# Performance work log

Hardware: AMD Instinct MI355X
Metric: run time of the kernel (lower is better)

## Reference

```python
import jax, jax.numpy as jnp
import numpy as np

B, S, P, D, H = 2, 1024, 1024, 2048, 16
DH = D // H
QMAX = 127.0


def quantize(x):
    # per-tensor abs-max int8 quantization, matching torch quantize(bits=8)
    scale = jnp.max(jnp.abs(x)) / QMAX
    x_q = jnp.clip(jnp.round(x / scale), -128.0, 127.0).astype(jnp.int8)
    return x_q, scale


def dequantize(x_q, scale):
    return x_q.astype(jnp.float32) * scale


def setup_inputs() -> dict:
    key = jax.random.key(0)
    ks = jax.random.split(key, 12)
    sd = 1.0 / np.sqrt(D)
    inp = {
        'hidden_states': jax.random.normal(ks[0], (B, S, D), jnp.float32),
        'Wq': jax.random.normal(ks[1], (D, D), jnp.float32) * sd,
        'bq': jnp.zeros((D,), jnp.float32),
        'Wk': jax.random.normal(ks[2], (D, D), jnp.float32) * sd,
        'bk': jnp.zeros((D,), jnp.float32),
        'Wv': jax.random.normal(ks[3], (D, D), jnp.float32) * sd,
        'bv': jnp.zeros((D,), jnp.float32),
        'Wo': jax.random.normal(ks[4], (D, D), jnp.float32) * sd,
        'bo': jnp.zeros((D,), jnp.float32),
        'past_k_q': jax.random.randint(ks[5], (B, P, D), -128, 128).astype(jnp.int8),
        'past_k_scale': jnp.float32(0.03),
        'past_v_q': jax.random.randint(ks[6], (B, P, D), -128, 128).astype(jnp.int8),
        'past_v_scale': jnp.float32(0.02),
    }
    return inp


def attention(h, k, v, Wq, bq, Wo, bo):
    # standard causal MHA; query positions are offset by the cache length P
    T = k.shape[1]  # P + S
    q = (h @ Wq + bq).reshape(B, S, H, DH)
    kh = k.reshape(B, T, H, DH)
    vh = v.reshape(B, T, H, DH)
    scores = jnp.einsum('bshd,bthd->bhst', q, kh) / np.sqrt(DH)  # [B,H,S,T]
    causal = jnp.arange(T)[None, :] <= (P + jnp.arange(S))[:, None]  # [S,T]
    scores = jnp.where(causal[None, None], scores, jnp.float32(-1e30))
    attn = jax.nn.softmax(scores, axis=-1)
    out = jnp.einsum('bhst,bthd->bshd', attn, vh).reshape(B, S, D)
    return out @ Wo + bo


def reference(hidden_states, Wq, bq, Wk, bk, Wv, bv, Wo, bo,
              past_k_q, past_k_scale, past_v_q, past_v_scale):
    k = hidden_states @ Wk + bk  # [B,S,D]
    v = hidden_states @ Wv + bv
    k_q, k_scale = quantize(k)
    v_q, v_scale = quantize(v)
    # dequantize cached KV and concat along the sequence dim (dim=1)
    k_prev = dequantize(past_k_q, past_k_scale)
    v_prev = dequantize(past_v_q, past_v_scale)
    k_full = jnp.concatenate([k_prev, k], axis=1)  # [B,P+S,D]
    v_full = jnp.concatenate([v_prev, v], axis=1)
    out = attention(hidden_states, k_full, v_full, Wq, bq, Wo, bo)
    return out, k_q, k_scale, v_q, v_scale
```

## Files before the change

### kernel.cpp

```cpp
#include <hip/hip_runtime.h>

#define SOFT_SCALE 0.08838834764831845f
#define BSD 4194304
#define NELEM 4194304

typedef __attribute__((ext_vector_type(4))) float    f32x4;
typedef __attribute__((ext_vector_type(8))) short    bf16x8;
typedef __attribute__((ext_vector_type(4))) short    bf16x4;
typedef __attribute__((ext_vector_type(4))) unsigned u32x4;

__device__ __forceinline__ float bs2f(short s) {
    unsigned u = ((unsigned)(unsigned short)s) << 16;
    return __builtin_bit_cast(float, u);
}
__device__ __forceinline__ short f2bs(float f) {
    unsigned u = __builtin_bit_cast(unsigned, f);
    unsigned r = (u + 0x7fffu + ((u >> 16) & 1u)) >> 16;
    return (short)r;
}

__device__ __forceinline__ void stage16(const short* g, short* l) {
#if __has_builtin(__builtin_amdgcn_global_load_lds)
    __builtin_amdgcn_global_load_lds(
        (const __attribute__((address_space(1))) void*)g,
        (__attribute__((address_space(3))) void*)l, 16, 0, 0);
#else
    *(bf16x8*)l = *(const bf16x8*)g;
#endif
}

__global__ void probe_init(const int* __restrict__ q, float* __restrict__ scal) {
    const int lane = threadIdx.x;
    int bad = 0;
#pragma unroll
    for (int i = 0; i < 4; ++i) {
        const int v = q[i * 64 + lane];
        bad |= (v < -128 || v > 127) ? 1 : 0;
    }
    const int anybad = __any(bad);
    if (lane == 0) ((int*)scal)[2] = anybad ? 0 : 1;
    if (lane == 1) scal[0] = 0.f;
    if (lane == 2) scal[1] = 0.f;
}

__global__ void prep_kernel(const float* __restrict__ X, short* __restrict__ Y,
                            const void* __restrict__ pk, const void* __restrict__ pv,
                            const float* __restrict__ psk, const float* __restrict__ psv,
                            short* __restrict__ Kf, short* __restrict__ Vf,
                            const int* __restrict__ wsflag) {
    const int z = blockIdx.z;
    const int stride = gridDim.x * blockDim.x;
    if (z == 0) {
        for (int i = blockIdx.x * blockDim.x + threadIdx.x; i < NELEM / 8; i += stride) {
            const int e = i * 8;
            f32x4 a = *(const f32x4*)&X[e];
            f32x4 b = *(const f32x4*)&X[e + 4];
            bf16x8 o;
            o[0] = f2bs(a[0]); o[1] = f2bs(a[1]); o[2] = f2bs(a[2]); o[3] = f2bs(a[3]);
            o[4] = f2bs(b[0]); o[5] = f2bs(b[1]); o[6] = f2bs(b[2]); o[7] = f2bs(b[3]);
            *(bf16x8*)&Y[e] = o;
        }
    } else {
        const void* src = (z == 2) ? pv : pk;
        const float sc = (z == 2) ? *psv : *psk;
        short* dst = (z == 2) ? Vf : Kf;
        const int flag = wsflag[2];
        for (int i = blockIdx.x * blockDim.x + threadIdx.x; i < NELEM / 8; i += stride) {
            const int e = i * 8;
            int vals[8];
            if (flag) {
                const int* s = (const int*)src + e;
                *(int4*)&vals[0] = *(const int4*)&s[0];
                *(int4*)&vals[4] = *(const int4*)&s[4];
            } else {
                const int2 wv = *(const int2*)((const char*)src + e);
#pragma unroll
                for (int j = 0; j < 4; ++j) vals[j] = (int)(signed char)(wv.x >> (8 * j));
#pragma unroll
                for (int j = 0; j < 4; ++j) vals[4 + j] = (int)(signed char)(wv.y >> (8 * j));
            }
            bf16x8 o;
#pragma unroll
            for (int j = 0; j < 8; ++j) o[j] = f2bs((float)vals[j] * sc);
            *(bf16x8*)&dst[e + ((e >> 21) << 21)] = o;
        }
    }
}

__global__ __launch_bounds__(256) void transpose_conv(const float* __restrict__ W0,
                                                      const float* __restrict__ W1,
                                                      const float* __restrict__ W2,
                                                      const float* __restrict__ W3,
                                                      short* __restrict__ WT) {
    __shared__ __align__(16) short Tl[64 * 68];
    const float* W = blockIdx.z == 0 ? W0 : (blockIdx.z == 1 ? W1 :
                     (blockIdx.z == 2 ? W2 : W3));
    short* out = WT + (long)blockIdx.z * 4194304;
    const int tid = threadIdx.x;
    const int n0 = blockIdx.x * 64, k0 = blockIdx.y * 64;
#pragma unroll
    for (int i = 0; i < 4; ++i) {
        const int e = i * 1024 + tid * 4;
        const int r = e >> 6, c = e & 63;
        f32x4 f = *(const f32x4*)&W[(long)(k0 + r) * 2048 + n0 + c];
        bf16x4 s4 = { f2bs(f[0]), f2bs(f[1]), f2bs(f[2]), f2bs(f[3]) };
        *(bf16x4*)&Tl[r * 68 + c] = s4;
    }
    __syncthreads();
#pragma unroll
    for (int i = 0; i < 4; ++i) {
        const int e = i * 1024 + tid * 4;
        const int nr = e >> 6, kk = e & 63;
        bf16x4 o = { Tl[(kk + 0) * 68 + nr], Tl[(kk + 1) * 68 + nr],
                     Tl[(kk + 2) * 68 + nr], Tl[(kk + 3) * 68 + nr] };
        *(bf16x4*)&out[(long)(n0 + nr) * 2048 + k0 + kk] = o;
    }
}

__global__ __launch_bounds__(256, 2) void gemm_m97(
    const short* __restrict__ A,
    const short* __restrict__ Bt0, const short* __restrict__ Bt1, const short* __restrict__ Bt2,
    const float* __restrict__ bi0, const float* __restrict__ bi1, const float* __restrict__ bi2,
    void* __restrict__ o0, void* __restrict__ o1, void* __restrict__ o2,
    int mode_sgl, float scale_sgl) {
    __shared__ __align__(16) short Al[2][4096];
    __shared__ __align__(16) short Bl[2][4096];
    const int nbx = gridDim.x, nby = gridDim.y, nbz = gridDim.z;
    const int nwg = nbx * nby * nbz;
    const int orig = blockIdx.x + nbx * (blockIdx.y + nby * blockIdx.z);
    const int cpx = nwg >> 3;
    int swz = (orig & 7) * cpx + (orig >> 3);
    const int bx = swz % nbx; swz /= nbx;
    const int by = swz % nby;
    const int bz = swz / nby;

    const short* Bt   = bz == 0 ? Bt0 : (bz == 1 ? Bt1 : Bt2);
    const float* bias = bz == 0 ? bi0 : (bz == 1 ? bi1 : bi2);
    void* outp        = bz == 0 ? o0  : (bz == 1 ? o1  : o2);
    int mode; float scl;
    if (nbz == 3) { mode = (bz == 0) ? 1 : 2; scl = (bz == 0) ? SOFT_SCALE : 1.f; }
    else          { mode = mode_sgl;          scl = scale_sgl; }

    const int tid = threadIdx.x, lane = tid & 63, w = tid >> 6;
    const int wm = w >> 1, wn = w & 1, l4 = lane >> 4, ln = lane & 15;
    const int m0 = by * 128, n0 = bx * 128;

    const short* gA0 = A  + (long)(m0 + (tid >> 2)) * 2048 + (tid & 3) * 8;
    const short* gA1 = gA0 + 64 * 2048;
    const short* gB0 = Bt + (long)(n0 + (tid >> 2)) * 2048 + (tid & 3) * 8;
    const short* gB1 = gB0 + 64 * 2048;

    f32x4 acc[4][4];
#pragma unroll
    for (int mi = 0; mi < 4; ++mi)
#pragma unroll
        for (int ni = 0; ni < 4; ++ni) acc[mi][ni] = (f32x4){0, 0, 0, 0};

#define STAGE_G(buf, ko)                                   \
    do {                                                   \
        stage16(gA0 + (ko), &Al[buf][tid * 8]);            \
        stage16(gA1 + (ko), &Al[buf][2048 + tid * 8]);     \
        stage16(gB0 + (ko), &Bl[buf][tid * 8]);            \
        stage16(gB1 + (ko), &Bl[buf][2048 + tid * 8]);     \
    } while (0)

    STAGE_G(0, 0);
    asm volatile("s_waitcnt vmcnt(0)" ::: "memory");
    __syncthreads();
    int cur = 0;
    for (int kt = 0; kt < 64; ++kt) {
        if (kt < 63) STAGE_G(cur ^ 1, (kt + 1) * 32);
        bf16x8 af[4], bfr[4];
#pragma unroll
        for (int mi = 0; mi < 4; ++mi)
            af[mi] = *(const bf16x8*)&Al[cur][(wm * 64 + mi * 16 + ln) * 32 + l4 * 8];
#pragma unroll
        for (int ni = 0; ni < 4; ++ni)
            bfr[ni] = *(const bf16x8*)&Bl[cur][(wn * 64 + ni * 16 + ln) * 32 + l4 * 8];
#pragma unroll
        for (int mi = 0; mi < 4; ++mi)
#pragma unroll
            for (int ni = 0; ni < 4; ++ni)
                acc[mi][ni] = __builtin_amdgcn_mfma_f32_16x16x32_bf16(
                    af[mi], bfr[ni], acc[mi][ni], 0, 0, 0);
        asm volatile("s_waitcnt vmcnt(0)" ::: "memory");
        __syncthreads();
        cur ^= 1;
    }
#undef STAGE_G

#pragma unroll
    for (int ni = 0; ni < 4; ++ni) {
        const int gn = n0 + wn * 64 + ni * 16 + ln;
        const float bv = bias[gn];
#pragma unroll
        for (int mi = 0; mi < 4; ++mi) {
#pragma unroll
            for (int r = 0; r < 4; ++r) {
                const int gm = m0 + wm * 64 + mi * 16 + l4 * 4 + r;
                const float v = (acc[mi][ni][r] + bv) * scl;
                if (mode == 0) {
                    ((float*)outp)[(long)gm * 2048 + gn] = v;
                } else if (mode == 1) {
                    ((short*)outp)[(long)gm * 2048 + gn] = f2bs(v);
                } else {
                    const int gr = gm + 1024 + ((gm >> 10) << 10);
                    ((short*)outp)[(long)gr * 2048 + gn] = f2bs(v);
                }
            }
        }
    }
}

__global__ __launch_bounds__(256, 2) void gemm_wo(const short* __restrict__ A,
                                                  const short* __restrict__ Bt,
                                                  const float* __restrict__ bias,
                                                  float* __restrict__ outp) {
    __shared__ __align__(16) short Al[2][4096];
    __shared__ __align__(16) short Bl[2][2048];
    const int orig = blockIdx.x + 32 * blockIdx.y;
    const int swz = (orig & 7) * 64 + (orig >> 3);
    const int bx = swz & 31, by = swz >> 5;
    const int tid = threadIdx.x, lane = tid & 63, w = tid >> 6;
    const int wm = w >> 1, wn = w & 1, l4 = lane >> 4, ln = lane & 15;
    const int m0 = by * 128, n0 = bx * 64;

    const short* gA0 = A  + (long)(m0 + (tid >> 2)) * 2048 + (tid & 3) * 8;
    const short* gA1 = gA0 + 64 * 2048;
    const short* gB0 = Bt + (long)(n0 + (tid >> 2)) * 2048 + (tid & 3) * 8;

    f32x4 acc[4][2];
#pragma unroll
    for (int mi = 0; mi < 4; ++mi)
#pragma unroll
        for (int ni = 0; ni < 2; ++ni) acc[mi][ni] = (f32x4){0, 0, 0, 0};

#define STAGE_W(buf, ko)                                   \
    do {                                                   \
        stage16(gA0 + (ko), &Al[buf][tid * 8]);            \
        stage16(gA1 + (ko), &Al[buf][2048 + tid * 8]);     \
        stage16(gB0 + (ko), &Bl[buf][tid * 8]);            \
    } while (0)

    STAGE_W(0, 0);
    asm volatile("s_waitcnt vmcnt(0)" ::: "memory");
    __syncthreads();
    int cur = 0;
    for (int kt = 0; kt < 64; ++kt) {
        if (kt < 63) STAGE_W(cur ^ 1, (kt + 1) * 32);
        bf16x8 af[4], bfr[2];
#pragma unroll
        for (int mi = 0; mi < 4; ++mi)
            af[mi] = *(const bf16x8*)&Al[cur][(wm * 64 + mi * 16 + ln) * 32 + l4 * 8];
#pragma unroll
        for (int ni = 0; ni < 2; ++ni)
            bfr[ni] = *(const bf16x8*)&Bl[cur][(wn * 32 + ni * 16 + ln) * 32 + l4 * 8];
#pragma unroll
        for (int mi = 0; mi < 4; ++mi)
#pragma unroll
            for (int ni = 0; ni < 2; ++ni)
                acc[mi][ni] = __builtin_amdgcn_mfma_f32_16x16x32_bf16(
                    af[mi], bfr[ni], acc[mi][ni], 0, 0, 0);
        asm volatile("s_waitcnt vmcnt(0)" ::: "memory");
        __syncthreads();
        cur ^= 1;
    }
#undef STAGE_W

#pragma unroll
    for (int ni = 0; ni < 2; ++ni) {
        const int gn = n0 + wn * 32 + ni * 16 + ln;
        const float bv = bias[gn];
#pragma unroll
        for (int mi = 0; mi < 4; ++mi) {
#pragma unroll
            for (int r = 0; r < 4; ++r) {
                const int gm = m0 + wm * 64 + mi * 16 + l4 * 4 + r;
                outp[(long)gm * 2048 + gn] = acc[mi][ni][r] + bv;
            }
        }
    }
}

__global__ void absmax_kernel(const short* __restrict__ Kf, const short* __restrict__ Vf,
                              float* __restrict__ scal) {
    const int z = blockIdx.z;
    const short* src = z ? Vf : Kf;
    const int tid = threadIdx.x, lane = tid & 63, w = tid >> 6;
    float mx = 0.f;
    const int stride = gridDim.x * blockDim.x;
    for (int i = blockIdx.x * blockDim.x + tid; i < NELEM / 8; i += stride) {
        const int e = i * 8;
        const int flat = e + 2097152 + ((e >> 21) << 21);
        bf16x8 v = *(const bf16x8*)&src[flat];
#pragma unroll
        for (int j = 0; j < 8; ++j) mx = fmaxf(mx, fabsf(bs2f(v[j])));
    }
#pragma unroll
    for (int o = 32; o > 0; o >>= 1) mx = fmaxf(mx, __shfl_xor(mx, o));
    __shared__ float wred[4];
    if (lane == 0) wred[w] = mx;
    __syncthreads();
    if (tid == 0) {
        const float m2 = fmaxf(fmaxf(wred[0], wred[1]), fmaxf(wred[2], wred[3]));
        atomicMax((unsigned int*)&scal[z], __builtin_bit_cast(unsigned int, m2));
    }
}

__global__ void quantize_kernel(const short* __restrict__ Kf, const short* __restrict__ Vf,
                                const float* __restrict__ scal, float* __restrict__ out) {
    const int z = blockIdx.z;
    const short* src = z ? Vf : Kf;
    const float mx = scal[z];
    const float scale = mx * (1.f / 127.f);
    const float inv = (mx > 0.f) ? 127.f / mx : 0.f;
    const long ob = z ? (2L * BSD + 1) : (1L * BSD);
    if (blockIdx.x == 0 && threadIdx.x == 0)
        out[z ? (3L * BSD + 1) : (2L * BSD)] = scale;
    const int stride = gridDim.x * blockDim.x;
    for (int i = blockIdx.x * blockDim.x + threadIdx.x; i < NELEM / 4; i += stride) {
        const int e = i * 4;
        const int flat = e + 2097152 + ((e >> 21) << 21);
        bf16x4 x4 = *(const bf16x4*)&src[flat];
        float4 q;
        q.x = fminf(127.f, fmaxf(-128.f, rintf(bs2f(x4[0]) * inv)));
        q.y = fminf(127.f, fmaxf(-128.f, rintf(bs2f(x4[1]) * inv)));
        q.z = fminf(127.f, fmaxf(-128.f, rintf(bs2f(x4[2]) * inv)));
        q.w = fminf(127.f, fmaxf(-128.f, rintf(bs2f(x4[3]) * inv)));
        *(float4*)&out[ob + e] = q;
    }
}

__global__ __launch_bounds__(256, 2) void attn_kernel(const short* __restrict__ Q,
                                                      const short* __restrict__ Kf,
                                                      const short* __restrict__ Vf,
                                                      short* __restrict__ O) {
    __shared__ __align__(16) short Kl[2][64 * 136];
    __shared__ __align__(16) short Vt[2][128 * 72];
    const int L = blockIdx.x + 16 * (blockIdx.y + 16 * blockIdx.z);
    const int x = L & 7, rr = L >> 3;
    const int qt0 = rr & 15, pgrp = rr >> 4;
    const int p = x + 8 * pgrp;
    const int h = p >> 1, b = p & 1;
    const int qt = (pgrp >= 2) ? (15 - qt0) : qt0;

    const int tid = threadIdx.x, w = tid >> 6, lane = tid & 63;
    const int l4 = lane >> 4, n = lane & 15;
    const int rg = tid >> 4, cg = tid & 15, stc = cg * 8;
    const int sIdx = qt * 64 + w * 16 + n;
    const int qlim = 1024 + sIdx;

    bf16x8 qf[4];
#pragma unroll
    for (int c = 0; c < 4; ++c)
        qf[c] = *(const bf16x8*)&Q[(long)(b * 1024 + sIdx) * 2048 + h * 128 + c * 32 + l4 * 8];

    f32x4 acco[8];
#pragma unroll
    for (int i = 0; i < 8; ++i) acco[i] = (f32x4){0, 0, 0, 0};
    float m_run = 0.f, l_run = 0.f;

    const short* Kb = Kf + (long)(b * 2048) * 2048 + h * 128;
    const short* Vb = Vf + (long)(b * 2048) * 2048 + h * 128;
    const int nt = 17 + qt;

    bf16x8 kreg[4], vreg[4];
#define LOAD_KV(te)                                                                   \
    do {                                                                              \
        _Pragma("unroll")                                                             \
        for (int i = 0; i < 4; ++i)                                                   \
            kreg[i] = *(const bf16x8*)&Kb[(long)((te) + i * 16 + rg) * 2048 + stc];   \
        _Pragma("unroll")                                                             \
        for (int i = 0; i < 4; ++i)                                                   \
            vreg[i] = *(const bf16x8*)&Vb[(long)((te) + rg * 4 + i) * 2048 + stc];    \
    } while (0)
#define WRITE_BUF(bf)                                                                 \
    do {                                                                              \
        _Pragma("unroll")                                                             \
        for (int i = 0; i < 4; ++i)                                                   \
            *(bf16x8*)&Kl[bf][(i * 16 + rg) * 136 + stc] = kreg[i];                   \
        _Pragma("unroll")                                                             \
        for (int j = 0; j < 8; ++j) {                                                 \
            const int d = stc + j;                                                    \
            bf16x4 c4 = { vreg[0][j], vreg[1][j], vreg[2][j], vreg[3][j] };           \
            *(bf16x4*)&Vt[bf][d * 72 + ((rg ^ ((d >> 3) & 7)) << 2)] = c4;            \
        }                                                                             \
    } while (0)

    LOAD_KV(0);
    WRITE_BUF(0);
    __syncthreads();

    for (int t = 0; t < nt; ++t) {
        const int buf = t & 1;
        const int t0 = t * 64;
        if (t + 1 < nt) LOAD_KV((t + 1) * 64);

        float p16[16];
        __builtin_amdgcn_s_setprio(1);
#pragma unroll
        for (int kt = 0; kt < 4; ++kt) {
            f32x4 sc4 = (f32x4){0, 0, 0, 0};
#pragma unroll
            for (int c = 0; c < 4; ++c) {
                bf16x8 kfr = *(const bf16x8*)&Kl[buf][(kt * 16 + n) * 136 + c * 32 + l4 * 8];
                sc4 = __builtin_amdgcn_mfma_f32_16x16x32_bf16(kfr, qf[c], sc4, 0, 0, 0);
            }
#pragma unroll
            for (int r = 0; r < 4; ++r) p16[kt * 4 + r] = sc4[r];
        }
        __builtin_amdgcn_s_setprio(0);
        if (t >= 16) {
#pragma unroll
            for (int i = 0; i < 16; ++i) {
                const int kg = t0 + (i >> 2) * 16 + l4 * 4 + (i & 3);
                if (kg > qlim) p16[i] = -1e30f;
            }
        }

        float tmax = fmaxf(p16[0], p16[1]);
#pragma unroll
        for (int i = 2; i < 16; ++i) tmax = fmaxf(tmax, p16[i]);
        tmax = fmaxf(tmax, __shfl_xor(tmax, 16));
        tmax = fmaxf(tmax, __shfl_xor(tmax, 32));
        float e16[16], tsum = 0.f;
#pragma unroll
        for (int i = 0; i < 16; ++i) { e16[i] = __expf(p16[i] - m_run); tsum += e16[i]; }
        if (!__all(tmax <= m_run + 8.f)) {
            const float mnew = fmaxf(m_run, tmax);
            const float fac = __expf(m_run - mnew);
            tsum *= fac;
#pragma unroll
            for (int i = 0; i < 16; ++i) e16[i] *= fac;
            l_run *= fac;
#pragma unroll
            for (int i = 0; i < 8; ++i) acco[i] *= fac;
            m_run = mnew;
        }
        tsum += __shfl_xor(tsum, 16);
        tsum += __shfl_xor(tsum, 32);
        l_run += tsum;

        u32x4 pw0, pw1;
#pragma unroll
        for (int wd = 0; wd < 4; ++wd) {
            unsigned r0, r1;
            asm("v_cvt_pk_bf16_f32 %0, %1, %2" : "=v"(r0) : "v"(e16[2 * wd]), "v"(e16[2 * wd + 1]));
            asm("v_cvt_pk_bf16_f32 %0, %1, %2" : "=v"(r1) : "v"(e16[8 + 2 * wd]), "v"(e16[8 + 2 * wd + 1]));
            pw0[wd] = r0; pw1[wd] = r1;
        }
        bf16x8 pb[2] = { __builtin_bit_cast(bf16x8, pw0), __builtin_bit_cast(bf16x8, pw1) };

        __builtin_amdgcn_s_setprio(1);
#pragma unroll
        for (int dc = 0; dc < 8; ++dc) {
            const int d = dc * 16 + n;
            const int swd = ((d >> 3) & 7) << 2;
#pragma unroll
            for (int k32 = 0; k32 < 2; ++k32) {
                bf16x4 g0 = *(const bf16x4*)&Vt[buf][d * 72 + (k32 * 32 + ((4 * l4) ^ swd))];
                bf16x4 g1 = *(const bf16x4*)&Vt[buf][d * 72 + (k32 * 32 + ((16 + 4 * l4) ^ swd))];
                bf16x8 vf = { g0[0], g0[1], g0[2], g0[3], g1[0], g1[1], g1[2], g1[3] };
                acco[dc] = __builtin_amdgcn_mfma_f32_16x16x32_bf16(vf, pb[k32], acco[dc], 0, 0, 0);
            }
        }
        __builtin_amdgcn_s_setprio(0);

        if (t + 1 < nt) WRITE_BUF(buf ^ 1);
        __syncthreads();
    }
#undef LOAD_KV
#undef WRITE_BUF

    const float inv = 1.f / l_run;
#pragma unroll
    for (int dc = 0; dc < 8; ++dc)
#pragma unroll
        for (int r = 0; r < 4; ++r)
            Kl[0][(w * 16 + n) * 136 + dc * 16 + l4 * 4 + r] = f2bs(acco[dc][r] * inv);
    __syncthreads();
#pragma unroll
    for (int i = 0; i < 4; ++i) {
        const int row = i * 4 + (lane >> 4);
        const int col = (lane & 15) * 8;
        bf16x8 ov = *(const bf16x8*)&Kl[0][(w * 16 + row) * 136 + col];
        *(bf16x8*)&O[(long)(b * 1024 + qt * 64 + w * 16 + row) * 2048 + h * 128 + col] = ov;
    }
}

extern "C" void kernel_launch(void* const* d_in, const int* in_sizes, int n_in,
                              void* d_out, int out_size, void* d_ws, size_t ws_size,
                              hipStream_t stream) {
    const float* h   = (const float*)d_in[0];
    const float* Wq  = (const float*)d_in[1];
    const float* bq  = (const float*)d_in[2];
    const float* Wk  = (const float*)d_in[3];
    const float* bk  = (const float*)d_in[4];
    const float* Wv  = (const float*)d_in[5];
    const float* bv  = (const float*)d_in[6];
    const float* Wo  = (const float*)d_in[7];
    const float* bo  = (const float*)d_in[8];
    const void*  pkq = d_in[9];
    const float* pks = (const float*)d_in[10];
    const void*  pvq = d_in[11];
    const float* pvs = (const float*)d_in[12];
    float* out = (float*)d_out;

    char* ws = (char*)d_ws;
    dim3 blk(256);

    if (ws_size >= 83886336ull) {
        float* scal  = (float*)ws;
        short* hbf   = (short*)(ws + 256);
        short* WT4   = (short*)(ws + 256 + 1L * 8388608);
        short* Qbf   = (short*)(ws + 256 + 5L * 8388608);
        short* Kfull = (short*)(ws + 256 + 6L * 8388608);
        short* Vfull = (short*)(ws + 256 + 6L * 8388608 + 16777216);
        short* attnb = hbf;

        probe_init<<<1, 64, 0, stream>>>((const int*)pkq, scal);
        prep_kernel<<<dim3(256, 1, 3), blk, 0, stream>>>(h, hbf, pkq, pvq, pks, pvs,
                                                         Kfull, Vfull, (const int*)d_ws);
        transpose_conv<<<dim3(32, 32, 4), blk, 0, stream>>>(Wq, Wk, Wv, Wo, WT4);
        gemm_m97<<<dim3(16, 16, 3), blk, 0, stream>>>(hbf, WT4, WT4 + 4194304, WT4 + 8388608,
                                                      bq, bk, bv, Qbf, Kfull, Vfull, 0, 1.f);
        absmax_kernel<<<dim3(512, 1, 2), blk, 0, stream>>>(Kfull, Vfull, scal);
        quantize_kernel<<<dim3(256, 1, 2), blk, 0, stream>>>(Kfull, Vfull, scal, out);
        attn_kernel<<<dim3(16, 16, 2), blk, 0, stream>>>(Qbf, Kfull, Vfull, attnb);
        gemm_wo<<<dim3(32, 16), blk, 0, stream>>>(attnb, WT4 + 12582912, bo, out);
    } else if (ws_size >= 75500000ull) {
        float* scal  = (float*)ws;
        short* hbf   = (short*)(ws + 256);
        short* WT3   = (short*)(ws + 256 + 1L * 8388608);
        short* Qbf   = (short*)(ws + 256 + 4L * 8388608);
        short* Kfull = (short*)(ws + 256 + 5L * 8388608);
        short* Vfull = (short*)(ws + 256 + 5L * 8388608 + 16777216);
        short* attnb = hbf;

        probe_init<<<1, 64, 0, stream>>>((const int*)pkq, scal);
        prep_kernel<<<dim3(256, 1, 3), blk, 0, stream>>>(h, hbf, pkq, pvq, pks, pvs,
                                                         Kfull, Vfull, (const int*)d_ws);
        transpose_conv<<<dim3(32, 32, 3), blk, 0, stream>>>(Wq, Wk, Wv, Wv, WT3);
        gemm_m97<<<dim3(16, 16, 3), blk, 0, stream>>>(hbf, WT3, WT3 + 4194304, WT3 + 8388608,
                                                      bq, bk, bv, Qbf, Kfull, Vfull, 0, 1.f);
        absmax_kernel<<<dim3(512, 1, 2), blk, 0, stream>>>(Kfull, Vfull, scal);
        quantize_kernel<<<dim3(256, 1, 2), blk, 0, stream>>>(Kfull, Vfull, scal, out);
        attn_kernel<<<dim3(16, 16, 2), blk, 0, stream>>>(Qbf, Kfull, Vfull, attnb);
        transpose_conv<<<dim3(32, 32, 1), blk, 0, stream>>>(Wo, Wo, Wo, Wo, WT3);
        gemm_wo<<<dim3(32, 16), blk, 0, stream>>>(attnb, WT3, bo, out);
    } else {
        float* scal  = (float*)ws;
        short* hbf   = (short*)(ws + 256);
        short* WT    = (short*)(ws + 256 + 1L * 8388608);
        short* Qbf   = (short*)(ws + 256 + 2L * 8388608);
        short* Kfull = (short*)(ws + 256 + 3L * 8388608);
        short* Vfull = (short*)(ws + 256 + 3L * 8388608 + 16777216);
        short* attnb = hbf;

        probe_init<<<1, 64, 0, stream>>>((const int*)pkq, scal);
        prep_kernel<<<dim3(256, 1, 3), blk, 0, stream>>>(h, hbf, pkq, pvq, pks, pvs,
                                                         Kfull, Vfull, (const int*)d_ws);
        transpose_conv<<<dim3(32, 32, 1), blk, 0, stream>>>(Wk, Wk, Wk, Wk, WT);
        gemm_m97<<<dim3(16, 16, 1), blk, 0, stream>>>(hbf, WT, WT, WT, bk, bk, bk,
                                                      Kfull, Kfull, Kfull, 2, 1.f);
        transpose_conv<<<dim3(32, 32, 1), blk, 0, stream>>>(Wv, Wv, Wv, Wv, WT);
        gemm_m97<<<dim3(16, 16, 1), blk, 0, stream>>>(hbf, WT, WT, WT, bv, bv, bv,
                                                      Vfull, Vfull, Vfull, 2, 1.f);
        absmax_kernel<<<dim3(512, 1, 2), blk, 0, stream>>>(Kfull, Vfull, scal);
        quantize_kernel<<<dim3(256, 1, 2), blk, 0, stream>>>(Kfull, Vfull, scal, out);
        transpose_conv<<<dim3(32, 32, 1), blk, 0, stream>>>(Wq, Wq, Wq, Wq, WT);
        gemm_m97<<<dim3(16, 16, 1), blk, 0, stream>>>(hbf, WT, WT, WT, bq, bq, bq,
                                                      Qbf, Qbf, Qbf, 1, SOFT_SCALE);
        attn_kernel<<<dim3(16, 16, 2), blk, 0, stream>>>(Qbf, Kfull, Vfull, attnb);
        transpose_conv<<<dim3(32, 32, 1), blk, 0, stream>>>(Wo, Wo, Wo, Wo, WT);
        gemm_wo<<<dim3(32, 16), blk, 0, stream>>>(attnb, WT, bo, out);
    }
}
```

Baseline: 221.6 us.

## Replace fused QKV GEMM with 256x256-tile, 512-thread register-prefetched kernel

```diff
diff --git a/kernel.cpp b/kernel.cpp
--- a/kernel.cpp
+++ b/kernel.cpp
@@ -117,29 +117,128 @@
     }
 }
 
-__global__ __launch_bounds__(256, 2) void gemm_m97(
+__global__ __launch_bounds__(512, 2) void gemm_qkv8(
     const short* __restrict__ A,
     const short* __restrict__ Bt0, const short* __restrict__ Bt1, const short* __restrict__ Bt2,
     const float* __restrict__ bi0, const float* __restrict__ bi1, const float* __restrict__ bi2,
-    void* __restrict__ o0, void* __restrict__ o1, void* __restrict__ o2,
-    int mode_sgl, float scale_sgl) {
-    __shared__ __align__(16) short Al[2][4096];
-    __shared__ __align__(16) short Bl[2][4096];
-    const int nbx = gridDim.x, nby = gridDim.y, nbz = gridDim.z;
-    const int nwg = nbx * nby * nbz;
-    const int orig = blockIdx.x + nbx * (blockIdx.y + nby * blockIdx.z);
-    const int cpx = nwg >> 3;
-    int swz = (orig & 7) * cpx + (orig >> 3);
-    const int bx = swz % nbx; swz /= nbx;
-    const int by = swz % nby;
-    const int bz = swz / nby;
+    void* __restrict__ o0, void* __restrict__ o1, void* __restrict__ o2) {
+    __shared__ __align__(16) short L[2][16384];
+
+    const int orig = blockIdx.x + 8 * (blockIdx.y + 8 * blockIdx.z);
+    int swz = (orig & 7) * 24 + (orig >> 3);
+    const int bx = swz & 7; swz >>= 3;
+    const int by = swz & 7;
+    const int bz = swz >> 3;
 
     const short* Bt   = bz == 0 ? Bt0 : (bz == 1 ? Bt1 : Bt2);
     const float* bias = bz == 0 ? bi0 : (bz == 1 ? bi1 : bi2);
     void* outp        = bz == 0 ? o0  : (bz == 1 ? o1  : o2);
-    int mode; float scl;
-    if (nbz == 3) { mode = (bz == 0) ? 1 : 2; scl = (bz == 0) ? SOFT_SCALE : 1.f; }
-    else          { mode = mode_sgl;          scl = scale_sgl; }
+    const int mode    = (bz == 0) ? 1 : 2;
+    const float scl   = (bz == 0) ? SOFT_SCALE : 1.f;
+
+    const int tid = threadIdx.x, lane = tid & 63, w = tid >> 6;
+    const int wm = w >> 2, wn = w & 3;
+    const int l4 = lane >> 4, ln = lane & 15;
+    const int m0 = by * 256, n0 = bx * 256;
+
+    const int srow = tid >> 2;
+    const int scol = (tid & 3) * 8;
+    const short* gA0 = A  + (long)(m0 + srow) * 2048 + scol;
+    const short* gA1 = A  + (long)(m0 + srow + 128) * 2048 + scol;
+    const short* gB0 = Bt + (long)(n0 + srow) * 2048 + scol;
+    const short* gB1 = Bt + (long)(n0 + srow + 128) * 2048 + scol;
+    const int w0 = srow * 32 + (scol ^ ((srow & 3) << 3));
+
+    const int aswz = (l4 * 8) ^ ((ln & 3) << 3);
+
+    f32x4 acc[8][4];
+#pragma unroll
+    for (int mi = 0; mi < 8; ++mi)
+#pragma unroll
+        for (int ni = 0; ni < 4; ++ni) acc[mi][ni] = (f32x4){0, 0, 0, 0};
+
+    bf16x8 g0, g1, g2, g3;
+#define LOADG(t)                                   \
+    do {                                           \
+        const int ko = (t) * 32;                   \
+        g0 = *(const bf16x8*)(gA0 + ko);           \
+        g1 = *(const bf16x8*)(gA1 + ko);           \
+        g2 = *(const bf16x8*)(gB0 + ko);           \
+        g3 = *(const bf16x8*)(gB1 + ko);           \
+    } while (0)
+#define WRITEL(c)                                  \
+    do {                                           \
+        *(bf16x8*)&L[c][w0] = g0;                  \
+        *(bf16x8*)&L[c][w0 + 4096] = g1;           \
+        *(bf16x8*)&L[c][8192 + w0] = g2;           \
+        *(bf16x8*)&L[c][8192 + w0 + 4096] = g3;    \
+    } while (0)
+
+    LOADG(0); WRITEL(0);
+    LOADG(1); WRITEL(1);
+    LOADG(2);
+    __syncthreads();
+
+    for (int s = 0; s < 64; ++s) {
+        const int c = s & 1;
+        bf16x8 af[8], bfq[4];
+#pragma unroll
+        for (int fm = 0; fm < 8; ++fm)
+            af[fm] = *(const bf16x8*)&L[c][(wm * 128 + fm * 16 + ln) * 32 + aswz];
+#pragma unroll
+        for (int fn = 0; fn < 4; ++fn)
+            bfq[fn] = *(const bf16x8*)&L[c][8192 + (wn * 64 + fn * 16 + ln) * 32 + aswz];
+        __builtin_amdgcn_s_setprio(1);
+#pragma unroll
+        for (int fm = 0; fm < 8; ++fm)
+#pragma unroll
+            for (int fn = 0; fn < 4; ++fn)
+                acc[fm][fn] = __builtin_amdgcn_mfma_f32_16x16x32_bf16(
+                    af[fm], bfq[fn], acc[fm][fn], 0, 0, 0);
+        __builtin_amdgcn_s_setprio(0);
+        asm volatile("s_waitcnt lgkmcnt(0)" ::: "memory");
+        __builtin_amdgcn_s_barrier();
+        if (s < 62) WRITEL(c);
+        if (s < 61) LOADG(s + 3);
+        asm volatile("s_waitcnt lgkmcnt(0)" ::: "memory");
+    }
+#undef LOADG
+#undef WRITEL
+
+#pragma unroll
+    for (int fn = 0; fn < 4; ++fn) {
+        const int gn = n0 + wn * 64 + fn * 16 + ln;
+        const float bv = bias[gn];
+#pragma unroll
+        for (int fm = 0; fm < 8; ++fm) {
+#pragma unroll
+            for (int r = 0; r < 4; ++r) {
+                const int gm = m0 + wm * 128 + fm * 16 + l4 * 4 + r;
+                const float v = (acc[fm][fn][r] + bv) * scl;
+                if (mode == 1) {
+                    ((short*)outp)[(long)gm * 2048 + gn] = f2bs(v);
+                } else {
+                    const int gr = gm + 1024 + ((gm >> 10) << 10);
+                    ((short*)outp)[(long)gr * 2048 + gn] = f2bs(v);
+                }
+            }
+        }
+    }
+}
+
+__global__ __launch_bounds__(256, 2) void gemm_m97(
+    const short* __restrict__ A, const short* __restrict__ Bt,
+    const float* __restrict__ bias, void* __restrict__ outp,
+    int mode, float scl) {
+    __shared__ __align__(16) short Al[2][4096];
+    __shared__ __align__(16) short Bl[2][4096];
+    const int nbx = gridDim.x, nby = gridDim.y;
+    const int nwg = nbx * nby;
+    const int orig = blockIdx.x + nbx * blockIdx.y;
+    const int cpx = nwg >> 3;
+    int swz = (orig & 7) * cpx + (orig >> 3);
+    const int bx = swz % nbx;
+    const int by = swz / nbx;
 
     const int tid = threadIdx.x, lane = tid & 63, w = tid >> 6;
     const int wm = w >> 1, wn = w & 1, l4 = lane >> 4, ln = lane & 15;
@@ -522,32 +621,13 @@
         prep_kernel<<<dim3(256, 1, 3), blk, 0, stream>>>(h, hbf, pkq, pvq, pks, pvs,
                                                          Kfull, Vfull, (const int*)d_ws);
         transpose_conv<<<dim3(32, 32, 4), blk, 0, stream>>>(Wq, Wk, Wv, Wo, WT4);
-        gemm_m97<<<dim3(16, 16, 3), blk, 0, stream>>>(hbf, WT4, WT4 + 4194304, WT4 + 8388608,
-                                                      bq, bk, bv, Qbf, Kfull, Vfull, 0, 1.f);
+        gemm_qkv8<<<dim3(8, 8, 3), dim3(512), 0, stream>>>(hbf, WT4, WT4 + 4194304,
+                                                           WT4 + 8388608, bq, bk, bv,
+                                                           Qbf, Kfull, Vfull);
         absmax_kernel<<<dim3(512, 1, 2), blk, 0, stream>>>(Kfull, Vfull, scal);
         quantize_kernel<<<dim3(256, 1, 2), blk, 0, stream>>>(Kfull, Vfull, scal, out);
         attn_kernel<<<dim3(16, 16, 2), blk, 0, stream>>>(Qbf, Kfull, Vfull, attnb);
         gemm_wo<<<dim3(32, 16), blk, 0, stream>>>(attnb, WT4 + 12582912, bo, out);
-    } else if (ws_size >= 75500000ull) {
-        float* scal  = (float*)ws;
-        short* hbf   = (short*)(ws + 256);
-        short* WT3   = (short*)(ws + 256 + 1L * 8388608);
-        short* Qbf   = (short*)(ws + 256 + 4L * 8388608);
-        short* Kfull = (short*)(ws + 256 + 5L * 8388608);
-        short* Vfull = (short*)(ws + 256 + 5L * 8388608 + 16777216);
-        short* attnb = hbf;
-
-        probe_init<<<1, 64, 0, stream>>>((const int*)pkq, scal);
-        prep_kernel<<<dim3(256, 1, 3), blk, 0, stream>>>(h, hbf, pkq, pvq, pks, pvs,
-                                                         Kfull, Vfull, (const int*)d_ws);
-        transpose_conv<<<dim3(32, 32, 3), blk, 0, stream>>>(Wq, Wk, Wv, Wv, WT3);
-        gemm_m97<<<dim3(16, 16, 3), blk, 0, stream>>>(hbf, WT3, WT3 + 4194304, WT3 + 8388608,
-                                                      bq, bk, bv, Qbf, Kfull, Vfull, 0, 1.f);
-        absmax_kernel<<<dim3(512, 1, 2), blk, 0, stream>>>(Kfull, Vfull, scal);
-        quantize_kernel<<<dim3(256, 1, 2), blk, 0, stream>>>(Kfull, Vfull, scal, out);
-        attn_kernel<<<dim3(16, 16, 2), blk, 0, stream>>>(Qbf, Kfull, Vfull, attnb);
-        transpose_conv<<<dim3(32, 32, 1), blk, 0, stream>>>(Wo, Wo, Wo, Wo, WT3);
-        gemm_wo<<<dim3(32, 16), blk, 0, stream>>>(attnb, WT3, bo, out);
     } else {
         float* scal  = (float*)ws;
         short* hbf   = (short*)(ws + 256);
@@ -561,16 +641,13 @@
         prep_kernel<<<dim3(256, 1, 3), blk, 0, stream>>>(h, hbf, pkq, pvq, pks, pvs,
                                                          Kfull, Vfull, (const int*)d_ws);
         transpose_conv<<<dim3(32, 32, 1), blk, 0, stream>>>(Wk, Wk, Wk, Wk, WT);
-        gemm_m97<<<dim3(16, 16, 1), blk, 0, stream>>>(hbf, WT, WT, WT, bk, bk, bk,
-                                                      Kfull, Kfull, Kfull, 2, 1.f);
+        gemm_m97<<<dim3(16, 16), blk, 0, stream>>>(hbf, WT, bk, Kfull, 2, 1.f);
         transpose_conv<<<dim3(32, 32, 1), blk, 0, stream>>>(Wv, Wv, Wv, Wv, WT);
-        gemm_m97<<<dim3(16, 16, 1), blk, 0, stream>>>(hbf, WT, WT, WT, bv, bv, bv,
-                                                      Vfull, Vfull, Vfull, 2, 1.f);
+        gemm_m97<<<dim3(16, 16), blk, 0, stream>>>(hbf, WT, bv, Vfull, 2, 1.f);
         absmax_kernel<<<dim3(512, 1, 2), blk, 0, stream>>>(Kfull, Vfull, scal);
         quantize_kernel<<<dim3(256, 1, 2), blk, 0, stream>>>(Kfull, Vfull, scal, out);
         transpose_conv<<<dim3(32, 32, 1), blk, 0, stream>>>(Wq, Wq, Wq, Wq, WT);
-        gemm_m97<<<dim3(16, 16, 1), blk, 0, stream>>>(hbf, WT, WT, WT, bq, bq, bq,
-                                                      Qbf, Qbf, Qbf, 1, SOFT_SCALE);
+        gemm_m97<<<dim3(16, 16), blk, 0, stream>>>(hbf, WT, bq, Qbf, 1, SOFT_SCALE);
         attn_kernel<<<dim3(16, 16, 2), blk, 0, stream>>>(Qbf, Kfull, Vfull, attnb);
         transpose_conv<<<dim3(32, 32, 1), blk, 0, stream>>>(Wo, Wo, Wo, Wo, WT);
         gemm_wo<<<dim3(32, 16), blk, 0, stream>>>(attnb, WT, bo, out);
```

Measured after the change: 219.0 us. No clear change (-1.2%).
